# Kernel tuning notes

Measured on AMD Instinct MI355X. Metric: run time of the kernel, lower is better.

Reference implementation:

```python
import jax, jax.numpy as jnp
import numpy as np

N_NODES = 100000
N_EDGES = 1600000
HIDDEN = 128
OUT = 64
NUM_LAYERS = 3


def setup_inputs() -> dict:
    key = jax.random.key(0)
    k1, k2, k3 = jax.random.split(key, 3)
    x = jax.random.normal(k1, (N_NODES, HIDDEN), dtype=jnp.float32)
    edge_index = jax.random.randint(k2, (2, N_EDGES), 0, N_NODES, dtype=jnp.int64)
    W = jax.random.normal(k3, (OUT, HIDDEN), dtype=jnp.float32) * (1.0 / np.sqrt(HIDDEN))
    b = jnp.zeros((OUT,), dtype=jnp.float32)
    return {"x": x, "edge_index": edge_index, "W": W, "b": b}


def reference(x, edge_index, W, b):
    n = x.shape[0]
    row, col = edge_index[0], edge_index[1]
    # degree of destination nodes (bincount over row), clamped to >= 1
    deg = jax.ops.segment_sum(jnp.ones_like(row, dtype=x.dtype), row, num_segments=n)
    deg_inv_sqrt = jnp.clip(deg, 1.0, None) ** -0.5
    norm = (deg_inv_sqrt[row] * deg_inv_sqrt[col])[:, None]  # [E, 1]

    def propagate(h):
        # gather -> scale -> scatter-add
        return jax.ops.segment_sum(h[col] * norm, row, num_segments=n)

    embs = [x]
    h = x
    for _ in range(NUM_LAYERS):
        h = propagate(h)
        embs.append(h)
    out = jnp.mean(jnp.stack(embs, axis=0), axis=0)  # [N, HIDDEN]
    return out @ W.T + b
```

## Files before the change

### kernel.cpp

```cpp
#include <hip/hip_runtime.h>

#define N_NODES 100000
#define N_EDGES 1600000
#define HIDDEN  128
#define OUTF    64
#define SLOT    48

#define EDGE4BLKS ((N_EDGES / 4 + 255) / 256)
#define NODEBLKS  ((N_NODES + 255) / 256)
#define PULLBLKS  ((N_NODES + 15) / 16)

__device__ __forceinline__ unsigned short f2bf(float f) {
    unsigned u = __float_as_uint(f);
    u += 0x7fffu + ((u >> 16) & 1u);
    return (unsigned short)(u >> 16);
}
__device__ __forceinline__ float2 bfp2f(unsigned p) {
    return make_float2(__uint_as_float(p << 16), __uint_as_float(p & 0xffff0000u));
}
__device__ __forceinline__ unsigned packbf(float a, float b) {
    return (unsigned)f2bf(a) | ((unsigned)f2bf(b) << 16);
}

__global__ void prep_kernel(const float* __restrict__ W, float* __restrict__ Wt,
                            int4* __restrict__ cnt4,
                            int4* __restrict__ z0d, int4* __restrict__ z1d,
                            int4* __restrict__ z2d) {
    int bid = blockIdx.x, tid = threadIdx.x;
    if (bid < 98) {
        int i = bid * 256 + tid;
        if (i < N_NODES / 4) cnt4[i] = make_int4(0, 0, 0, 0);
    } else if (bid < 130) {
        int i = (bid - 98) * 256 + tid;
        if (i < HIDDEN * OUTF) {
            int o = i / HIDDEN, k = i % HIDDEN;
            Wt[k * OUTF + o] = W[i];
        }
    } else {
        if (tid < 8)       z0d[tid]      = make_int4(0, 0, 0, 0);
        else if (tid < 16) z1d[tid - 8]  = make_int4(0, 0, 0, 0);
        else if (tid < 24) z2d[tid - 16] = make_int4(0, 0, 0, 0);
    }
}

#define GR    64
#define BK    32
#define HSP   36
#define WTP   68
__global__ __launch_bounds__(256) void mega_a_kernel(const float* __restrict__ x,
                                                     const float* __restrict__ Wt,
                                                     unsigned short* __restrict__ y0,
                                                     const int* __restrict__ ei,
                                                     int* __restrict__ cnt,
                                                     int* __restrict__ rank) {
    __shared__ float hs[GR * HSP];
    __shared__ float wt[BK * WTP];
    int tid = threadIdx.x;

    if (blockIdx.x & 1) {
        int cb = blockIdx.x >> 1;
        int t  = cb * 256 + tid;
        int e0 = t * 4;
        if (e0 + 3 < N_EDGES) {
            int4 r4 = *(const int4*)(ei + e0);
            int k0 = atomicAdd(&cnt[r4.x], 1);
            int k1 = atomicAdd(&cnt[r4.y], 1);
            int k2 = atomicAdd(&cnt[r4.z], 1);
            int k3 = atomicAdd(&cnt[r4.w], 1);
            *(int4*)(rank + e0) = make_int4(k0, k1, k2, k3);
        } else {
            for (int e = e0; e < N_EDGES; ++e) rank[e] = atomicAdd(&cnt[ei[e]], 1);
        }
        return;
    }

    int rowBase = (blockIdx.x >> 1) * GR;
    int o4 = (tid & 15) * 4;
    int rq = (tid >> 4) * 4;
    float4 a0 = {0,0,0,0}, a1 = {0,0,0,0}, a2 = {0,0,0,0}, a3 = {0,0,0,0};

    for (int kt = 0; kt < HIDDEN / BK; ++kt) {
        if (kt) __syncthreads();
        int kbase = kt * BK;
        #pragma unroll
        for (int t = 0; t < 2; ++t) {
            int f = tid + t * 256;
            int r = f >> 3, c4 = (f & 7) * 4;
            int row = rowBase + r;
            float4 v = (row < N_NODES) ? *(const float4*)(x + (size_t)row * HIDDEN + kbase + c4)
                                       : make_float4(0.f, 0.f, 0.f, 0.f);
            *(float4*)&hs[r * HSP + c4] = v;
        }
        #pragma unroll
        for (int t = 0; t < 2; ++t) {
            int f = tid + t * 256;
            int k = f >> 4, c4 = (f & 15) * 4;
            float4 v = *(const float4*)(Wt + (size_t)(kbase + k) * OUTF + c4);
            *(float4*)&wt[k * WTP + c4] = v;
        }
        __syncthreads();
        #pragma unroll 8
        for (int kk = 0; kk < BK; ++kk) {
            float4 wv = *(const float4*)&wt[kk * WTP + o4];
            float h0 = hs[(rq + 0) * HSP + kk];
            float h1 = hs[(rq + 1) * HSP + kk];
            float h2 = hs[(rq + 2) * HSP + kk];
            float h3 = hs[(rq + 3) * HSP + kk];
            a0.x += h0 * wv.x; a0.y += h0 * wv.y; a0.z += h0 * wv.z; a0.w += h0 * wv.w;
            a1.x += h1 * wv.x; a1.y += h1 * wv.y; a1.z += h1 * wv.z; a1.w += h1 * wv.w;
            a2.x += h2 * wv.x; a2.y += h2 * wv.y; a2.z += h2 * wv.z; a2.w += h2 * wv.w;
            a3.x += h3 * wv.x; a3.y += h3 * wv.y; a3.z += h3 * wv.z; a3.w += h3 * wv.w;
        }
    }
    int row = rowBase + rq;
    #pragma unroll
    for (int r = 0; r < 4; ++r) {
        if (row + r < N_NODES) {
            float4 a = (r == 0) ? a0 : (r == 1) ? a1 : (r == 2) ? a2 : a3;
            ushort4 s = {f2bf(a.x), f2bf(a.y), f2bf(a.z), f2bf(a.w)};
            *(ushort4*)&y0[(size_t)(row + r) * OUTF + o4] = s;
        }
    }
}

__global__ void mega_b_kernel(const int* __restrict__ ei,
                              const int* __restrict__ rank,
                              int* __restrict__ csr,
                              const int* __restrict__ cnt,
                              float* __restrict__ dinv,
                              float* __restrict__ rdinv) {
    int bid = blockIdx.x, tid = threadIdx.x;
    if (bid < EDGE4BLKS) {
        int t  = bid * 256 + tid;
        int e0 = t * 4;
        if (e0 + 3 < N_EDGES) {
            int4 r4 = *(const int4*)(ei + e0);
            int4 c4 = *(const int4*)(ei + N_EDGES + e0);
            int4 k4 = *(const int4*)(rank + e0);
            if (k4.x < SLOT) csr[r4.x * SLOT + k4.x] = c4.x;
            if (k4.y < SLOT) csr[r4.y * SLOT + k4.y] = c4.y;
            if (k4.z < SLOT) csr[r4.z * SLOT + k4.z] = c4.z;
            if (k4.w < SLOT) csr[r4.w * SLOT + k4.w] = c4.w;
        } else {
            for (int e = e0; e < N_EDGES; ++e) {
                int k = rank[e];
                if (k < SLOT) csr[ei[e] * SLOT + k] = ei[N_EDGES + e];
            }
        }
    } else {
        int i = (bid - EDGE4BLKS) * 256 + tid;
        if (i < N_NODES) {
            int deg  = cnt[i];
            float d  = fmaxf((float)deg, 1.0f);
            dinv[i]  = rsqrtf(d);
            rdinv[i] = sqrtf(d);
            if (i == 0) dinv[N_NODES] = 0.0f;
            int dc = deg > SLOT ? SLOT : deg;
            int dp = (dc + 7) & ~7;
            #pragma unroll
            for (int j = 0; j < 7; ++j)
                if (dc + j < dp) csr[i * SLOT + dc + j] = N_NODES;
        }
    }
}

template<bool SC>
__global__ __launch_bounds__(256) void pull_v2_kernel(const int* __restrict__ cnt,
                                                      const int* __restrict__ csr,
                                                      const float* __restrict__ dinv,
                                                      const unsigned short* __restrict__ zsrc,
                                                      unsigned short* __restrict__ zdst) {
    int lane = threadIdx.x & 63;
    int wid  = (blockIdx.x * blockDim.x + threadIdx.x) >> 6;
    int g    = lane >> 3;
    int node = wid * 4 + (g >> 1);
    int par  = g & 1;
    int fo   = (lane & 7) * 8;
    bool valid = node < N_NODES;
    int deg = valid ? cnt[node] : 0;
    if (deg > SLOT) deg = SLOT;
    int degp = (deg + 7) & ~7;
    int s = node * SLOT;
    float a0=0.f,a1=0.f,a2=0.f,a3=0.f,a4=0.f,a5=0.f,a6=0.f,a7=0.f;

    int e16 = degp & ~15;
    int i = 0;
    for (; i < e16; i += 16) {
        int c0 = csr[s + i +  0 + par];
        int c1 = csr[s + i +  2 + par];
        int c2 = csr[s + i +  4 + par];
        int c3 = csr[s + i +  6 + par];
        int c4 = csr[s + i +  8 + par];
        int c5 = csr[s + i + 10 + par];
        int c6 = csr[s + i + 12 + par];
        int c7 = csr[s + i + 14 + par];
        float d0=1.f,d1=1.f,d2=1.f,d3=1.f,d4=1.f,d5=1.f,d6=1.f,d7=1.f;
        if (SC) {
            d0 = dinv[c0]; d1 = dinv[c1]; d2 = dinv[c2]; d3 = dinv[c3];
            d4 = dinv[c4]; d5 = dinv[c5]; d6 = dinv[c6]; d7 = dinv[c7];
        }
        uint4 p0 = *(const uint4*)(zsrc + (size_t)c0 * OUTF + fo);
        uint4 p1 = *(const uint4*)(zsrc + (size_t)c1 * OUTF + fo);
        uint4 p2 = *(const uint4*)(zsrc + (size_t)c2 * OUTF + fo);
        uint4 p3 = *(const uint4*)(zsrc + (size_t)c3 * OUTF + fo);
        uint4 p4 = *(const uint4*)(zsrc + (size_t)c4 * OUTF + fo);
        uint4 p5 = *(const uint4*)(zsrc + (size_t)c5 * OUTF + fo);
        uint4 p6 = *(const uint4*)(zsrc + (size_t)c6 * OUTF + fo);
        uint4 p7 = *(const uint4*)(zsrc + (size_t)c7 * OUTF + fo);
        #define ACC(P, D) { \
            float2 q0 = bfp2f(P.x), q1 = bfp2f(P.y), q2 = bfp2f(P.z), q3 = bfp2f(P.w); \
            a0 += D*q0.x; a1 += D*q0.y; a2 += D*q1.x; a3 += D*q1.y; \
            a4 += D*q2.x; a5 += D*q2.y; a6 += D*q3.x; a7 += D*q3.y; }
        ACC(p0, d0) ACC(p1, d1) ACC(p2, d2) ACC(p3, d3)
        ACC(p4, d4) ACC(p5, d5) ACC(p6, d6) ACC(p7, d7)
    }
    if (degp & 8) {
        int c0 = csr[s + i + 0 + par];
        int c1 = csr[s + i + 2 + par];
        int c2 = csr[s + i + 4 + par];
        int c3 = csr[s + i + 6 + par];
        float d0=1.f,d1=1.f,d2=1.f,d3=1.f;
        if (SC) { d0 = dinv[c0]; d1 = dinv[c1]; d2 = dinv[c2]; d3 = dinv[c3]; }
        uint4 p0 = *(const uint4*)(zsrc + (size_t)c0 * OUTF + fo);
        uint4 p1 = *(const uint4*)(zsrc + (size_t)c1 * OUTF + fo);
        uint4 p2 = *(const uint4*)(zsrc + (size_t)c2 * OUTF + fo);
        uint4 p3 = *(const uint4*)(zsrc + (size_t)c3 * OUTF + fo);
        ACC(p0, d0) ACC(p1, d1) ACC(p2, d2) ACC(p3, d3)
        #undef ACC
    }
    a0 += __shfl_xor(a0, 8); a1 += __shfl_xor(a1, 8);
    a2 += __shfl_xor(a2, 8); a3 += __shfl_xor(a3, 8);
    a4 += __shfl_xor(a4, 8); a5 += __shfl_xor(a5, 8);
    a6 += __shfl_xor(a6, 8); a7 += __shfl_xor(a7, 8);
    if ((lane & 8) == 0 && valid) {
        float dn = dinv[node];
        float zs = dn * dn;
        uint4 o;
        o.x = packbf(a0 * zs, a1 * zs);
        o.y = packbf(a2 * zs, a3 * zs);
        o.z = packbf(a4 * zs, a5 * zs);
        o.w = packbf(a6 * zs, a7 * zs);
        *(uint4*)(zdst + (size_t)node * OUTF + fo) = o;
    }
}

__global__ __launch_bounds__(256) void pull_merge_v2_kernel(const int* __restrict__ cnt,
                                                            const int* __restrict__ csr,
                                                            const float* __restrict__ dinv,
                                                            const float* __restrict__ rdinv,
                                                            const unsigned short* __restrict__ y0,
                                                            const unsigned short* __restrict__ z1,
                                                            const unsigned short* __restrict__ z2,
                                                            const float* __restrict__ b,
                                                            float* __restrict__ out) {
    int lane = threadIdx.x & 63;
    int wid  = (blockIdx.x * blockDim.x + threadIdx.x) >> 6;
    int g    = lane >> 3;
    int node = wid * 4 + (g >> 1);
    int par  = g & 1;
    int fo   = (lane & 7) * 8;
    bool valid = node < N_NODES;
    int deg = valid ? cnt[node] : 0;
    if (deg > SLOT) deg = SLOT;
    int degp = (deg + 7) & ~7;
    int s = node * SLOT;
    float a0=0.f,a1=0.f,a2=0.f,a3=0.f,a4=0.f,a5=0.f,a6=0.f,a7=0.f;

    int e16 = degp & ~15;
    int i = 0;
    for (; i < e16; i += 16) {
        int c0 = csr[s + i +  0 + par];
        int c1 = csr[s + i +  2 + par];
        int c2 = csr[s + i +  4 + par];
        int c3 = csr[s + i +  6 + par];
        int c4 = csr[s + i +  8 + par];
        int c5 = csr[s + i + 10 + par];
        int c6 = csr[s + i + 12 + par];
        int c7 = csr[s + i + 14 + par];
        uint4 p0 = *(const uint4*)(z2 + (size_t)c0 * OUTF + fo);
        uint4 p1 = *(const uint4*)(z2 + (size_t)c1 * OUTF + fo);
        uint4 p2 = *(const uint4*)(z2 + (size_t)c2 * OUTF + fo);
        uint4 p3 = *(const uint4*)(z2 + (size_t)c3 * OUTF + fo);
        uint4 p4 = *(const uint4*)(z2 + (size_t)c4 * OUTF + fo);
        uint4 p5 = *(const uint4*)(z2 + (size_t)c5 * OUTF + fo);
        uint4 p6 = *(const uint4*)(z2 + (size_t)c6 * OUTF + fo);
        uint4 p7 = *(const uint4*)(z2 + (size_t)c7 * OUTF + fo);
        #define ACC1(P) { \
            float2 q0 = bfp2f(P.x), q1 = bfp2f(P.y), q2 = bfp2f(P.z), q3 = bfp2f(P.w); \
            a0 += q0.x; a1 += q0.y; a2 += q1.x; a3 += q1.y; \
            a4 += q2.x; a5 += q2.y; a6 += q3.x; a7 += q3.y; }
        ACC1(p0) ACC1(p1) ACC1(p2) ACC1(p3) ACC1(p4) ACC1(p5) ACC1(p6) ACC1(p7)
    }
    if (degp & 8) {
        int c0 = csr[s + i + 0 + par];
        int c1 = csr[s + i + 2 + par];
        int c2 = csr[s + i + 4 + par];
        int c3 = csr[s + i + 6 + par];
        uint4 p0 = *(const uint4*)(z2 + (size_t)c0 * OUTF + fo);
        uint4 p1 = *(const uint4*)(z2 + (size_t)c1 * OUTF + fo);
        uint4 p2 = *(const uint4*)(z2 + (size_t)c2 * OUTF + fo);
        uint4 p3 = *(const uint4*)(z2 + (size_t)c3 * OUTF + fo);
        ACC1(p0) ACC1(p1) ACC1(p2) ACC1(p3)
        #undef ACC1
    }
    a0 += __shfl_xor(a0, 8); a1 += __shfl_xor(a1, 8);
    a2 += __shfl_xor(a2, 8); a3 += __shfl_xor(a3, 8);
    a4 += __shfl_xor(a4, 8); a5 += __shfl_xor(a5, 8);
    a6 += __shfl_xor(a6, 8); a7 += __shfl_xor(a7, 8);
    if ((lane & 8) == 0 && valid) {
        size_t idx = (size_t)node * OUTF + fo;
        float dn = dinv[node];
        float rd = rdinv[node];
        uint4 py = *(const uint4*)(y0 + idx);
        uint4 pz1 = *(const uint4*)(z1 + idx);
        uint4 pz2 = *(const uint4*)(z2 + idx);
        float4 bv0 = *(const float4*)(b + fo);
        float4 bv1 = *(const float4*)(b + fo + 4);
        float2 y_0 = bfp2f(py.x), y_1 = bfp2f(py.y), y_2 = bfp2f(py.z), y_3 = bfp2f(py.w);
        float2 u_0 = bfp2f(pz1.x), u_1 = bfp2f(pz1.y), u_2 = bfp2f(pz1.z), u_3 = bfp2f(pz1.w);
        float2 v_0 = bfp2f(pz2.x), v_1 = bfp2f(pz2.y), v_2 = bfp2f(pz2.z), v_3 = bfp2f(pz2.w);
        float4 r0, r1;
        r0.x = 0.25f * ((dn * y_0.x + u_0.x + v_0.x) * rd + dn * a0) + bv0.x;
        r0.y = 0.25f * ((dn * y_0.y + u_0.y + v_0.y) * rd + dn * a1) + bv0.y;
        r0.z = 0.25f * ((dn * y_1.x + u_1.x + v_1.x) * rd + dn * a2) + bv0.z;
        r0.w = 0.25f * ((dn * y_1.y + u_1.y + v_1.y) * rd + dn * a3) + bv0.w;
        r1.x = 0.25f * ((dn * y_2.x + u_2.x + v_2.x) * rd + dn * a4) + bv1.x;
        r1.y = 0.25f * ((dn * y_2.y + u_2.y + v_2.y) * rd + dn * a5) + bv1.y;
        r1.z = 0.25f * ((dn * y_3.x + u_3.x + v_3.x) * rd + dn * a6) + bv1.z;
        r1.w = 0.25f * ((dn * y_3.y + u_3.y + v_3.y) * rd + dn * a7) + bv1.w;
        *(float4*)(out + idx) = r0;
        *(float4*)(out + idx + 4) = r1;
    }
}

extern "C" void kernel_launch(void* const* d_in, const int* in_sizes, int n_in,
                              void* d_out, int out_size, void* d_ws, size_t ws_size,
                              hipStream_t stream) {
    const float* x  = (const float*)d_in[0];
    const int*   ei = (const int*)d_in[1];
    const float* W  = (const float*)d_in[2];
    const float* b  = (const float*)d_in[3];
    float*       out = (float*)d_out;

    const size_t ZROWS = (size_t)N_NODES + 1;
    unsigned short* y0 = (unsigned short*)d_ws;
    unsigned short* z1 = y0 + ZROWS * OUTF;
    unsigned short* z2 = z1 + ZROWS * OUTF;
    float* Wt      = (float*)(z2 + ZROWS * OUTF);
    int*   csr     = (int*)(Wt + HIDDEN * OUTF);
    int*   cnt     = csr + (size_t)N_NODES * SLOT;
    float* dinv    = (float*)(cnt + N_NODES);
    float* rdinv   = dinv + (N_NODES + 1);

    int* rank = (int*)z2;

    const int BLK = 256;

    prep_kernel<<<131, BLK, 0, stream>>>(W, Wt, (int4*)cnt,
                                         (int4*)(y0 + (size_t)N_NODES * OUTF),
                                         (int4*)(z1 + (size_t)N_NODES * OUTF),
                                         (int4*)(z2 + (size_t)N_NODES * OUTF));
    mega_a_kernel<<<2 * EDGE4BLKS, BLK, 0, stream>>>(x, Wt, y0, ei, cnt, rank);
    mega_b_kernel<<<EDGE4BLKS + NODEBLKS, BLK, 0, stream>>>(ei, rank, csr, cnt, dinv, rdinv);
    pull_v2_kernel<true><<<PULLBLKS, BLK, 0, stream>>>(cnt, csr, dinv, y0, z1);
    pull_v2_kernel<false><<<PULLBLKS, BLK, 0, stream>>>(cnt, csr, dinv, z1, z2);
    pull_merge_v2_kernel<<<PULLBLKS, BLK, 0, stream>>>(cnt, csr, dinv, rdinv,
                                                       y0, z1, z2, b, out);
}
```

Measured before the change: 282.3 us.

## Split feature matrices into 16-column quarter planes for cache-local gathers

Stores the bf16 node feature arrays as four separate planes of 16 features each (32 bytes per row), and launches the pull kernels over four times as many blocks, one feature quarter per block group. Each gather pass then touches a working set a quarter the size, which is meant to fit better in L2/MALL and cut DRAM traffic for random neighbor reads. In exchange the CSR indices and degrees are re-read four times, each gather moves only 32 bytes per row, and the shuffle reduction grows to three steps. The rank scratch now aliases z1 instead of z2, and the first pull kernel re-zeroes the sentinel row of z1 that this aliasing overwrites.

```diff
diff --git a/kernel.cpp b/kernel.cpp
--- a/kernel.cpp
+++ b/kernel.cpp
@@ -8,7 +8,8 @@
 
 #define EDGE4BLKS ((N_EDGES / 4 + 255) / 256)
 #define NODEBLKS  ((N_NODES + 255) / 256)
-#define PULLBLKS  ((N_NODES + 15) / 16)
+#define QSTRIDE ((size_t)(N_NODES + 1) * 16)
+#define T_TILES ((N_NODES + 15) / 16)
 
 __device__ __forceinline__ unsigned short f2bf(float f) {
     unsigned u = __float_as_uint(f);
@@ -24,8 +25,9 @@
 
 __global__ void prep_kernel(const float* __restrict__ W, float* __restrict__ Wt,
                             int4* __restrict__ cnt4,
-                            int4* __restrict__ z0d, int4* __restrict__ z1d,
-                            int4* __restrict__ z2d) {
+                            unsigned short* __restrict__ y0,
+                            unsigned short* __restrict__ z1,
+                            unsigned short* __restrict__ z2) {
     int bid = blockIdx.x, tid = threadIdx.x;
     if (bid < 98) {
         int i = bid * 256 + tid;
@@ -37,9 +39,13 @@
             Wt[k * OUTF + o] = W[i];
         }
     } else {
-        if (tid < 8)       z0d[tid]      = make_int4(0, 0, 0, 0);
-        else if (tid < 16) z1d[tid - 8]  = make_int4(0, 0, 0, 0);
-        else if (tid < 24) z2d[tid - 16] = make_int4(0, 0, 0, 0);
+        if (tid < 24) {
+            unsigned short* base = (tid < 8) ? y0 : (tid < 16) ? z1 : z2;
+            int r = tid & 7;
+            int q = r >> 1, part = r & 1;
+            int4* p = (int4*)(base + q * QSTRIDE + (size_t)N_NODES * 16);
+            p[part] = make_int4(0, 0, 0, 0);
+        }
     }
 }
 
@@ -113,12 +119,14 @@
         }
     }
     int row = rowBase + rq;
+    int q   = o4 >> 4;
+    int off = o4 & 15;
     #pragma unroll
     for (int r = 0; r < 4; ++r) {
         if (row + r < N_NODES) {
             float4 a = (r == 0) ? a0 : (r == 1) ? a1 : (r == 2) ? a2 : a3;
             ushort4 s = {f2bf(a.x), f2bf(a.y), f2bf(a.z), f2bf(a.w)};
-            *(ushort4*)&y0[(size_t)(row + r) * OUTF + o4] = s;
+            *(ushort4*)&y0[q * QSTRIDE + (size_t)(row + r) * 16 + off] = s;
         }
     }
 }
@@ -164,75 +172,62 @@
     }
 }
 
-template<bool SC>
-__global__ __launch_bounds__(256) void pull_v2_kernel(const int* __restrict__ cnt,
-                                                      const int* __restrict__ csr,
-                                                      const float* __restrict__ dinv,
-                                                      const unsigned short* __restrict__ zsrc,
-                                                      unsigned short* __restrict__ zdst) {
+template<bool SC, bool FIXZ>
+__global__ __launch_bounds__(256) void pull_q_kernel(const int* __restrict__ cnt,
+                                                     const int* __restrict__ csr,
+                                                     const float* __restrict__ dinv,
+                                                     const unsigned short* __restrict__ zsrc,
+                                                     unsigned short* __restrict__ zdst) {
+    if (FIXZ && blockIdx.x == 0 && threadIdx.x < 2)
+        ((int4*)(zdst + (size_t)N_NODES * 16))[threadIdx.x] = make_int4(0, 0, 0, 0);
+    int q    = blockIdx.x / T_TILES;
+    int t    = blockIdx.x % T_TILES;
     int lane = threadIdx.x & 63;
-    int wid  = (blockIdx.x * blockDim.x + threadIdx.x) >> 6;
-    int g    = lane >> 3;
-    int node = wid * 4 + (g >> 1);
-    int par  = g & 1;
-    int fo   = (lane & 7) * 8;
+    int wv   = threadIdx.x >> 6;
+    int n    = lane >> 4;
+    int slot = (lane >> 1) & 7;
+    int h    = lane & 1;
+    int node = t * 16 + wv * 4 + n;
     bool valid = node < N_NODES;
     int deg = valid ? cnt[node] : 0;
     if (deg > SLOT) deg = SLOT;
     int degp = (deg + 7) & ~7;
     int s = node * SLOT;
+    const unsigned short* zq = zsrc + q * QSTRIDE;
+    int fo = h * 8;
     float a0=0.f,a1=0.f,a2=0.f,a3=0.f,a4=0.f,a5=0.f,a6=0.f,a7=0.f;
 
     int e16 = degp & ~15;
     int i = 0;
+    #define ACC(P, D) { \
+        float2 q0 = bfp2f(P.x), q1 = bfp2f(P.y), q2 = bfp2f(P.z), q3 = bfp2f(P.w); \
+        a0 += D*q0.x; a1 += D*q0.y; a2 += D*q1.x; a3 += D*q1.y; \
+        a4 += D*q2.x; a5 += D*q2.y; a6 += D*q3.x; a7 += D*q3.y; }
     for (; i < e16; i += 16) {
-        int c0 = csr[s + i +  0 + par];
-        int c1 = csr[s + i +  2 + par];
-        int c2 = csr[s + i +  4 + par];
-        int c3 = csr[s + i +  6 + par];
-        int c4 = csr[s + i +  8 + par];
-        int c5 = csr[s + i + 10 + par];
-        int c6 = csr[s + i + 12 + par];
-        int c7 = csr[s + i + 14 + par];
-        float d0=1.f,d1=1.f,d2=1.f,d3=1.f,d4=1.f,d5=1.f,d6=1.f,d7=1.f;
-        if (SC) {
-            d0 = dinv[c0]; d1 = dinv[c1]; d2 = dinv[c2]; d3 = dinv[c3];
-            d4 = dinv[c4]; d5 = dinv[c5]; d6 = dinv[c6]; d7 = dinv[c7];
-        }
-        uint4 p0 = *(const uint4*)(zsrc + (size_t)c0 * OUTF + fo);
-        uint4 p1 = *(const uint4*)(zsrc + (size_t)c1 * OUTF + fo);
-        uint4 p2 = *(const uint4*)(zsrc + (size_t)c2 * OUTF + fo);
-        uint4 p3 = *(const uint4*)(zsrc + (size_t)c3 * OUTF + fo);
-        uint4 p4 = *(const uint4*)(zsrc + (size_t)c4 * OUTF + fo);
-        uint4 p5 = *(const uint4*)(zsrc + (size_t)c5 * OUTF + fo);
-        uint4 p6 = *(const uint4*)(zsrc + (size_t)c6 * OUTF + fo);
-        uint4 p7 = *(const uint4*)(zsrc + (size_t)c7 * OUTF + fo);
-        #define ACC(P, D) { \
-            float2 q0 = bfp2f(P.x), q1 = bfp2f(P.y), q2 = bfp2f(P.z), q3 = bfp2f(P.w); \
-            a0 += D*q0.x; a1 += D*q0.y; a2 += D*q1.x; a3 += D*q1.y; \
-            a4 += D*q2.x; a5 += D*q2.y; a6 += D*q3.x; a7 += D*q3.y; }
-        ACC(p0, d0) ACC(p1, d1) ACC(p2, d2) ACC(p3, d3)
-        ACC(p4, d4) ACC(p5, d5) ACC(p6, d6) ACC(p7, d7)
+        int c0 = csr[s + i + slot];
+        int c1 = csr[s + i + 8 + slot];
+        float d0 = 1.f, d1 = 1.f;
+        if (SC) { d0 = dinv[c0]; d1 = dinv[c1]; }
+        uint4 p0 = *(const uint4*)(zq + (size_t)c0 * 16 + fo);
+        uint4 p1 = *(const uint4*)(zq + (size_t)c1 * 16 + fo);
+        ACC(p0, d0) ACC(p1, d1)
     }
     if (degp & 8) {
-        int c0 = csr[s + i + 0 + par];
-        int c1 = csr[s + i + 2 + par];
-        int c2 = csr[s + i + 4 + par];
-        int c3 = csr[s + i + 6 + par];
-        float d0=1.f,d1=1.f,d2=1.f,d3=1.f;
-        if (SC) { d0 = dinv[c0]; d1 = dinv[c1]; d2 = dinv[c2]; d3 = dinv[c3]; }
-        uint4 p0 = *(const uint4*)(zsrc + (size_t)c0 * OUTF + fo);
-        uint4 p1 = *(const uint4*)(zsrc + (size_t)c1 * OUTF + fo);
-        uint4 p2 = *(const uint4*)(zsrc + (size_t)c2 * OUTF + fo);
-        uint4 p3 = *(const uint4*)(zsrc + (size_t)c3 * OUTF + fo);
-        ACC(p0, d0) ACC(p1, d1) ACC(p2, d2) ACC(p3, d3)
-        #undef ACC
-    }
-    a0 += __shfl_xor(a0, 8); a1 += __shfl_xor(a1, 8);
-    a2 += __shfl_xor(a2, 8); a3 += __shfl_xor(a3, 8);
-    a4 += __shfl_xor(a4, 8); a5 += __shfl_xor(a5, 8);
-    a6 += __shfl_xor(a6, 8); a7 += __shfl_xor(a7, 8);
-    if ((lane & 8) == 0 && valid) {
+        int c0 = csr[s + i + slot];
+        float d0 = 1.f;
+        if (SC) d0 = dinv[c0];
+        uint4 p0 = *(const uint4*)(zq + (size_t)c0 * 16 + fo);
+        ACC(p0, d0)
+    }
+    #undef ACC
+    #pragma unroll
+    for (int m = 2; m <= 8; m <<= 1) {
+        a0 += __shfl_xor(a0, m); a1 += __shfl_xor(a1, m);
+        a2 += __shfl_xor(a2, m); a3 += __shfl_xor(a3, m);
+        a4 += __shfl_xor(a4, m); a5 += __shfl_xor(a5, m);
+        a6 += __shfl_xor(a6, m); a7 += __shfl_xor(a7, m);
+    }
+    if (slot == 0 && valid) {
         float dn = dinv[node];
         float zs = dn * dn;
         uint4 o;
@@ -240,83 +235,73 @@
         o.y = packbf(a2 * zs, a3 * zs);
         o.z = packbf(a4 * zs, a5 * zs);
         o.w = packbf(a6 * zs, a7 * zs);
-        *(uint4*)(zdst + (size_t)node * OUTF + fo) = o;
-    }
-}
-
-__global__ __launch_bounds__(256) void pull_merge_v2_kernel(const int* __restrict__ cnt,
-                                                            const int* __restrict__ csr,
-                                                            const float* __restrict__ dinv,
-                                                            const float* __restrict__ rdinv,
-                                                            const unsigned short* __restrict__ y0,
-                                                            const unsigned short* __restrict__ z1,
-                                                            const unsigned short* __restrict__ z2,
-                                                            const float* __restrict__ b,
-                                                            float* __restrict__ out) {
+        *(uint4*)(zdst + q * QSTRIDE + (size_t)node * 16 + fo) = o;
+    }
+}
+
+__global__ __launch_bounds__(256) void pull_merge_q_kernel(const int* __restrict__ cnt,
+                                                           const int* __restrict__ csr,
+                                                           const float* __restrict__ dinv,
+                                                           const float* __restrict__ rdinv,
+                                                           const unsigned short* __restrict__ y0,
+                                                           const unsigned short* __restrict__ z1,
+                                                           const unsigned short* __restrict__ z2,
+                                                           const float* __restrict__ b,
+                                                           float* __restrict__ out) {
+    int q    = blockIdx.x / T_TILES;
+    int t    = blockIdx.x % T_TILES;
     int lane = threadIdx.x & 63;
-    int wid  = (blockIdx.x * blockDim.x + threadIdx.x) >> 6;
-    int g    = lane >> 3;
-    int node = wid * 4 + (g >> 1);
-    int par  = g & 1;
-    int fo   = (lane & 7) * 8;
+    int wv   = threadIdx.x >> 6;
+    int n    = lane >> 4;
+    int slot = (lane >> 1) & 7;
+    int h    = lane & 1;
+    int node = t * 16 + wv * 4 + n;
     bool valid = node < N_NODES;
     int deg = valid ? cnt[node] : 0;
     if (deg > SLOT) deg = SLOT;
     int degp = (deg + 7) & ~7;
     int s = node * SLOT;
+    const unsigned short* zq = z2 + q * QSTRIDE;
+    int fo = h * 8;
     float a0=0.f,a1=0.f,a2=0.f,a3=0.f,a4=0.f,a5=0.f,a6=0.f,a7=0.f;
 
     int e16 = degp & ~15;
     int i = 0;
+    #define ACC1(P) { \
+        float2 q0 = bfp2f(P.x), q1 = bfp2f(P.y), q2 = bfp2f(P.z), q3 = bfp2f(P.w); \
+        a0 += q0.x; a1 += q0.y; a2 += q1.x; a3 += q1.y; \
+        a4 += q2.x; a5 += q2.y; a6 += q3.x; a7 += q3.y; }
     for (; i < e16; i += 16) {
-        int c0 = csr[s + i +  0 + par];
-        int c1 = csr[s + i +  2 + par];
-        int c2 = csr[s + i +  4 + par];
-        int c3 = csr[s + i +  6 + par];
-        int c4 = csr[s + i +  8 + par];
-        int c5 = csr[s + i + 10 + par];
-        int c6 = csr[s + i + 12 + par];
-        int c7 = csr[s + i + 14 + par];
-        uint4 p0 = *(const uint4*)(z2 + (size_t)c0 * OUTF + fo);
-        uint4 p1 = *(const uint4*)(z2 + (size_t)c1 * OUTF + fo);
-        uint4 p2 = *(const uint4*)(z2 + (size_t)c2 * OUTF + fo);
-        uint4 p3 = *(const uint4*)(z2 + (size_t)c3 * OUTF + fo);
-        uint4 p4 = *(const uint4*)(z2 + (size_t)c4 * OUTF + fo);
-        uint4 p5 = *(const uint4*)(z2 + (size_t)c5 * OUTF + fo);
-        uint4 p6 = *(const uint4*)(z2 + (size_t)c6 * OUTF + fo);
-        uint4 p7 = *(const uint4*)(z2 + (size_t)c7 * OUTF + fo);
-        #define ACC1(P) { \
-            float2 q0 = bfp2f(P.x), q1 = bfp2f(P.y), q2 = bfp2f(P.z), q3 = bfp2f(P.w); \
-            a0 += q0.x; a1 += q0.y; a2 += q1.x; a3 += q1.y; \
-            a4 += q2.x; a5 += q2.y; a6 += q3.x; a7 += q3.y; }
-        ACC1(p0) ACC1(p1) ACC1(p2) ACC1(p3) ACC1(p4) ACC1(p5) ACC1(p6) ACC1(p7)
+        int c0 = csr[s + i + slot];
+        int c1 = csr[s + i + 8 + slot];
+        uint4 p0 = *(const uint4*)(zq + (size_t)c0 * 16 + fo);
+        uint4 p1 = *(const uint4*)(zq + (size_t)c1 * 16 + fo);
+        ACC1(p0) ACC1(p1)
     }
     if (degp & 8) {
-        int c0 = csr[s + i + 0 + par];
-        int c1 = csr[s + i + 2 + par];
-        int c2 = csr[s + i + 4 + par];
-        int c3 = csr[s + i + 6 + par];
-        uint4 p0 = *(const uint4*)(z2 + (size_t)c0 * OUTF + fo);
-        uint4 p1 = *(const uint4*)(z2 + (size_t)c1 * OUTF + fo);
-        uint4 p2 = *(const uint4*)(z2 + (size_t)c2 * OUTF + fo);
-        uint4 p3 = *(const uint4*)(z2 + (size_t)c3 * OUTF + fo);
-        ACC1(p0) ACC1(p1) ACC1(p2) ACC1(p3)
-        #undef ACC1
-    }
-    a0 += __shfl_xor(a0, 8); a1 += __shfl_xor(a1, 8);
-    a2 += __shfl_xor(a2, 8); a3 += __shfl_xor(a3, 8);
-    a4 += __shfl_xor(a4, 8); a5 += __shfl_xor(a5, 8);
-    a6 += __shfl_xor(a6, 8); a7 += __shfl_xor(a7, 8);
-    if ((lane & 8) == 0 && valid) {
-        size_t idx = (size_t)node * OUTF + fo;
+        int c0 = csr[s + i + slot];
+        uint4 p0 = *(const uint4*)(zq + (size_t)c0 * 16 + fo);
+        ACC1(p0)
+    }
+    #undef ACC1
+    #pragma unroll
+    for (int m = 2; m <= 8; m <<= 1) {
+        a0 += __shfl_xor(a0, m); a1 += __shfl_xor(a1, m);
+        a2 += __shfl_xor(a2, m); a3 += __shfl_xor(a3, m);
+        a4 += __shfl_xor(a4, m); a5 += __shfl_xor(a5, m);
+        a6 += __shfl_xor(a6, m); a7 += __shfl_xor(a7, m);
+    }
+    if (slot == 0 && valid) {
+        size_t idxq = q * QSTRIDE + (size_t)node * 16 + fo;
         float dn = dinv[node];
         float rd = rdinv[node];
-        uint4 py = *(const uint4*)(y0 + idx);
-        uint4 pz1 = *(const uint4*)(z1 + idx);
-        uint4 pz2 = *(const uint4*)(z2 + idx);
-        float4 bv0 = *(const float4*)(b + fo);
-        float4 bv1 = *(const float4*)(b + fo + 4);
-        float2 y_0 = bfp2f(py.x), y_1 = bfp2f(py.y), y_2 = bfp2f(py.z), y_3 = bfp2f(py.w);
+        uint4 py  = *(const uint4*)(y0 + idxq);
+        uint4 pz1 = *(const uint4*)(z1 + idxq);
+        uint4 pz2 = *(const uint4*)(z2 + idxq);
+        int fb = q * 16 + fo;
+        float4 bv0 = *(const float4*)(b + fb);
+        float4 bv1 = *(const float4*)(b + fb + 4);
+        float2 y_0 = bfp2f(py.x),  y_1 = bfp2f(py.y),  y_2 = bfp2f(py.z),  y_3 = bfp2f(py.w);
         float2 u_0 = bfp2f(pz1.x), u_1 = bfp2f(pz1.y), u_2 = bfp2f(pz1.z), u_3 = bfp2f(pz1.w);
         float2 v_0 = bfp2f(pz2.x), v_1 = bfp2f(pz2.y), v_2 = bfp2f(pz2.z), v_3 = bfp2f(pz2.w);
         float4 r0, r1;
@@ -328,8 +313,9 @@
         r1.y = 0.25f * ((dn * y_2.y + u_2.y + v_2.y) * rd + dn * a5) + bv1.y;
         r1.z = 0.25f * ((dn * y_3.x + u_3.x + v_3.x) * rd + dn * a6) + bv1.z;
         r1.w = 0.25f * ((dn * y_3.y + u_3.y + v_3.y) * rd + dn * a7) + bv1.w;
-        *(float4*)(out + idx) = r0;
-        *(float4*)(out + idx + 4) = r1;
+        size_t oi = (size_t)node * OUTF + fb;
+        *(float4*)(out + oi)     = r0;
+        *(float4*)(out + oi + 4) = r1;
     }
 }
 
@@ -342,28 +328,24 @@
     const float* b  = (const float*)d_in[3];
     float*       out = (float*)d_out;
 
-    const size_t ZROWS = (size_t)N_NODES + 1;
     unsigned short* y0 = (unsigned short*)d_ws;
-    unsigned short* z1 = y0 + ZROWS * OUTF;
-    unsigned short* z2 = z1 + ZROWS * OUTF;
-    float* Wt      = (float*)(z2 + ZROWS * OUTF);
+    unsigned short* z1 = y0 + 4 * QSTRIDE;
+    unsigned short* z2 = z1 + 4 * QSTRIDE;
+    float* Wt      = (float*)(z2 + 4 * QSTRIDE);
     int*   csr     = (int*)(Wt + HIDDEN * OUTF);
     int*   cnt     = csr + (size_t)N_NODES * SLOT;
     float* dinv    = (float*)(cnt + N_NODES);
     float* rdinv   = dinv + (N_NODES + 1);
 
-    int* rank = (int*)z2;
+    int* rank = (int*)z1;
 
     const int BLK = 256;
 
-    prep_kernel<<<131, BLK, 0, stream>>>(W, Wt, (int4*)cnt,
-                                         (int4*)(y0 + (size_t)N_NODES * OUTF),
-                                         (int4*)(z1 + (size_t)N_NODES * OUTF),
-                                         (int4*)(z2 + (size_t)N_NODES * OUTF));
+    prep_kernel<<<131, BLK, 0, stream>>>(W, Wt, (int4*)cnt, y0, z1, z2);
     mega_a_kernel<<<2 * EDGE4BLKS, BLK, 0, stream>>>(x, Wt, y0, ei, cnt, rank);
     mega_b_kernel<<<EDGE4BLKS + NODEBLKS, BLK, 0, stream>>>(ei, rank, csr, cnt, dinv, rdinv);
-    pull_v2_kernel<true><<<PULLBLKS, BLK, 0, stream>>>(cnt, csr, dinv, y0, z1);
-    pull_v2_kernel<false><<<PULLBLKS, BLK, 0, stream>>>(cnt, csr, dinv, z1, z2);
-    pull_merge_v2_kernel<<<PULLBLKS, BLK, 0, stream>>>(cnt, csr, dinv, rdinv,
-                                                       y0, z1, z2, b, out);
-}
+    pull_q_kernel<true, true><<<4 * T_TILES, BLK, 0, stream>>>(cnt, csr, dinv, y0, z1);
+    pull_q_kernel<false, false><<<4 * T_TILES, BLK, 0, stream>>>(cnt, csr, dinv, z1, z2);
+    pull_merge_q_kernel<<<4 * T_TILES, BLK, 0, stream>>>(cnt, csr, dinv, rdinv,
+                                                         y0, z1, z2, b, out);
+}
```

Result: slower. 366.4 us (+29.8%).

## Assign two nodes per 8-lane group in pull kernels instead of splitting one node

Applied to the files above, without the earlier changes.

Each 8-lane group now processes two destination nodes with interleaved gathers and no cross-lane reduction, where before two groups split one node's edges by parity. Each thread issues 16 independent row loads per iteration, which raises memory-level parallelism and removes the shuffle reduction. The launch uses a quarter as many blocks. The cost is more registers per thread, possibly lower occupancy, and idle padded loads when the two nodes have unequal degrees.

```diff
diff --git a/kernel.cpp b/kernel.cpp
--- a/kernel.cpp
+++ b/kernel.cpp
@@ -8,7 +8,7 @@
 
 #define EDGE4BLKS ((N_EDGES / 4 + 255) / 256)
 #define NODEBLKS  ((N_NODES + 255) / 256)
-#define PULLBLKS  ((N_NODES + 15) / 16)
+#define PULLBLKS  ((N_NODES + 63) / 64)
 
 __device__ __forceinline__ unsigned short f2bf(float f) {
     unsigned u = __float_as_uint(f);
@@ -165,7 +165,7 @@
 }
 
 template<bool SC>
-__global__ __launch_bounds__(256) void pull_v2_kernel(const int* __restrict__ cnt,
+__global__ __launch_bounds__(256) void pull_v3_kernel(const int* __restrict__ cnt,
                                                       const int* __restrict__ csr,
                                                       const float* __restrict__ dinv,
                                                       const unsigned short* __restrict__ zsrc,
@@ -173,78 +173,93 @@
     int lane = threadIdx.x & 63;
     int wid  = (blockIdx.x * blockDim.x + threadIdx.x) >> 6;
     int g    = lane >> 3;
-    int node = wid * 4 + (g >> 1);
-    int par  = g & 1;
     int fo   = (lane & 7) * 8;
-    bool valid = node < N_NODES;
-    int deg = valid ? cnt[node] : 0;
-    if (deg > SLOT) deg = SLOT;
-    int degp = (deg + 7) & ~7;
-    int s = node * SLOT;
-    float a0=0.f,a1=0.f,a2=0.f,a3=0.f,a4=0.f,a5=0.f,a6=0.f,a7=0.f;
-
-    int e16 = degp & ~15;
-    int i = 0;
-    for (; i < e16; i += 16) {
-        int c0 = csr[s + i +  0 + par];
-        int c1 = csr[s + i +  2 + par];
-        int c2 = csr[s + i +  4 + par];
-        int c3 = csr[s + i +  6 + par];
-        int c4 = csr[s + i +  8 + par];
-        int c5 = csr[s + i + 10 + par];
-        int c6 = csr[s + i + 12 + par];
-        int c7 = csr[s + i + 14 + par];
-        float d0=1.f,d1=1.f,d2=1.f,d3=1.f,d4=1.f,d5=1.f,d6=1.f,d7=1.f;
+    int nodeA = wid * 16 + g * 2;
+    int nodeB = nodeA + 1;
+    bool vA = nodeA < N_NODES, vB = nodeB < N_NODES;
+    int degA = vA ? cnt[nodeA] : 0; if (degA > SLOT) degA = SLOT;
+    int degB = vB ? cnt[nodeB] : 0; if (degB > SLOT) degB = SLOT;
+    int dpA = (degA + 7) & ~7;
+    int dpB = (degB + 7) & ~7;
+    int sA = nodeA * SLOT, sB = nodeB * SLOT;
+    int nIt = (dpA > dpB ? dpA : dpB);
+    float aA0=0.f,aA1=0.f,aA2=0.f,aA3=0.f,aA4=0.f,aA5=0.f,aA6=0.f,aA7=0.f;
+    float aB0=0.f,aB1=0.f,aB2=0.f,aB3=0.f,aB4=0.f,aB5=0.f,aB6=0.f,aB7=0.f;
+
+    for (int j = 0; j < nIt; j += 8) {
+        bool doA = j < dpA, doB = j < dpB;
+        int cA0,cA1,cA2,cA3,cA4,cA5,cA6,cA7;
+        int cB0,cB1,cB2,cB3,cB4,cB5,cB6,cB7;
+        if (doA) {
+            cA0 = csr[sA+j+0]; cA1 = csr[sA+j+1]; cA2 = csr[sA+j+2]; cA3 = csr[sA+j+3];
+            cA4 = csr[sA+j+4]; cA5 = csr[sA+j+5]; cA6 = csr[sA+j+6]; cA7 = csr[sA+j+7];
+        } else { cA0=cA1=cA2=cA3=cA4=cA5=cA6=cA7=N_NODES; }
+        if (doB) {
+            cB0 = csr[sB+j+0]; cB1 = csr[sB+j+1]; cB2 = csr[sB+j+2]; cB3 = csr[sB+j+3];
+            cB4 = csr[sB+j+4]; cB5 = csr[sB+j+5]; cB6 = csr[sB+j+6]; cB7 = csr[sB+j+7];
+        } else { cB0=cB1=cB2=cB3=cB4=cB5=cB6=cB7=N_NODES; }
+        uint4 pA0 = *(const uint4*)(zsrc + (size_t)cA0 * OUTF + fo);
+        uint4 pA1 = *(const uint4*)(zsrc + (size_t)cA1 * OUTF + fo);
+        uint4 pA2 = *(const uint4*)(zsrc + (size_t)cA2 * OUTF + fo);
+        uint4 pA3 = *(const uint4*)(zsrc + (size_t)cA3 * OUTF + fo);
+        uint4 pA4 = *(const uint4*)(zsrc + (size_t)cA4 * OUTF + fo);
+        uint4 pA5 = *(const uint4*)(zsrc + (size_t)cA5 * OUTF + fo);
+        uint4 pA6 = *(const uint4*)(zsrc + (size_t)cA6 * OUTF + fo);
+        uint4 pA7 = *(const uint4*)(zsrc + (size_t)cA7 * OUTF + fo);
+        uint4 pB0 = *(const uint4*)(zsrc + (size_t)cB0 * OUTF + fo);
+        uint4 pB1 = *(const uint4*)(zsrc + (size_t)cB1 * OUTF + fo);
+        uint4 pB2 = *(const uint4*)(zsrc + (size_t)cB2 * OUTF + fo);
+        uint4 pB3 = *(const uint4*)(zsrc + (size_t)cB3 * OUTF + fo);
+        uint4 pB4 = *(const uint4*)(zsrc + (size_t)cB4 * OUTF + fo);
+        uint4 pB5 = *(const uint4*)(zsrc + (size_t)cB5 * OUTF + fo);
+        uint4 pB6 = *(const uint4*)(zsrc + (size_t)cB6 * OUTF + fo);
+        uint4 pB7 = *(const uint4*)(zsrc + (size_t)cB7 * OUTF + fo);
+        float dA0=1.f,dA1=1.f,dA2=1.f,dA3=1.f,dA4=1.f,dA5=1.f,dA6=1.f,dA7=1.f;
+        float dB0=1.f,dB1=1.f,dB2=1.f,dB3=1.f,dB4=1.f,dB5=1.f,dB6=1.f,dB7=1.f;
         if (SC) {
-            d0 = dinv[c0]; d1 = dinv[c1]; d2 = dinv[c2]; d3 = dinv[c3];
-            d4 = dinv[c4]; d5 = dinv[c5]; d6 = dinv[c6]; d7 = dinv[c7];
-        }
-        uint4 p0 = *(const uint4*)(zsrc + (size_t)c0 * OUTF + fo);
-        uint4 p1 = *(const uint4*)(zsrc + (size_t)c1 * OUTF + fo);
-        uint4 p2 = *(const uint4*)(zsrc + (size_t)c2 * OUTF + fo);
-        uint4 p3 = *(const uint4*)(zsrc + (size_t)c3 * OUTF + fo);
-        uint4 p4 = *(const uint4*)(zsrc + (size_t)c4 * OUTF + fo);
-        uint4 p5 = *(const uint4*)(zsrc + (size_t)c5 * OUTF + fo);
-        uint4 p6 = *(const uint4*)(zsrc + (size_t)c6 * OUTF + fo);
-        uint4 p7 = *(const uint4*)(zsrc + (size_t)c7 * OUTF + fo);
-        #define ACC(P, D) { \
+            dA0 = dinv[cA0]; dA1 = dinv[cA1]; dA2 = dinv[cA2]; dA3 = dinv[cA3];
+            dA4 = dinv[cA4]; dA5 = dinv[cA5]; dA6 = dinv[cA6]; dA7 = dinv[cA7];
+            dB0 = dinv[cB0]; dB1 = dinv[cB1]; dB2 = dinv[cB2]; dB3 = dinv[cB3];
+            dB4 = dinv[cB4]; dB5 = dinv[cB5]; dB6 = dinv[cB6]; dB7 = dinv[cB7];
+        }
+        #define ACCA(P, D) { \
             float2 q0 = bfp2f(P.x), q1 = bfp2f(P.y), q2 = bfp2f(P.z), q3 = bfp2f(P.w); \
-            a0 += D*q0.x; a1 += D*q0.y; a2 += D*q1.x; a3 += D*q1.y; \
-            a4 += D*q2.x; a5 += D*q2.y; a6 += D*q3.x; a7 += D*q3.y; }
-        ACC(p0, d0) ACC(p1, d1) ACC(p2, d2) ACC(p3, d3)
-        ACC(p4, d4) ACC(p5, d5) ACC(p6, d6) ACC(p7, d7)
-    }
-    if (degp & 8) {
-        int c0 = csr[s + i + 0 + par];
-        int c1 = csr[s + i + 2 + par];
-        int c2 = csr[s + i + 4 + par];
-        int c3 = csr[s + i + 6 + par];
-        float d0=1.f,d1=1.f,d2=1.f,d3=1.f;
-        if (SC) { d0 = dinv[c0]; d1 = dinv[c1]; d2 = dinv[c2]; d3 = dinv[c3]; }
-        uint4 p0 = *(const uint4*)(zsrc + (size_t)c0 * OUTF + fo);
-        uint4 p1 = *(const uint4*)(zsrc + (size_t)c1 * OUTF + fo);
-        uint4 p2 = *(const uint4*)(zsrc + (size_t)c2 * OUTF + fo);
-        uint4 p3 = *(const uint4*)(zsrc + (size_t)c3 * OUTF + fo);
-        ACC(p0, d0) ACC(p1, d1) ACC(p2, d2) ACC(p3, d3)
-        #undef ACC
-    }
-    a0 += __shfl_xor(a0, 8); a1 += __shfl_xor(a1, 8);
-    a2 += __shfl_xor(a2, 8); a3 += __shfl_xor(a3, 8);
-    a4 += __shfl_xor(a4, 8); a5 += __shfl_xor(a5, 8);
-    a6 += __shfl_xor(a6, 8); a7 += __shfl_xor(a7, 8);
-    if ((lane & 8) == 0 && valid) {
-        float dn = dinv[node];
+            aA0 += D*q0.x; aA1 += D*q0.y; aA2 += D*q1.x; aA3 += D*q1.y; \
+            aA4 += D*q2.x; aA5 += D*q2.y; aA6 += D*q3.x; aA7 += D*q3.y; }
+        #define ACCB(P, D) { \
+            float2 q0 = bfp2f(P.x), q1 = bfp2f(P.y), q2 = bfp2f(P.z), q3 = bfp2f(P.w); \
+            aB0 += D*q0.x; aB1 += D*q0.y; aB2 += D*q1.x; aB3 += D*q1.y; \
+            aB4 += D*q2.x; aB5 += D*q2.y; aB6 += D*q3.x; aB7 += D*q3.y; }
+        ACCA(pA0,dA0) ACCA(pA1,dA1) ACCA(pA2,dA2) ACCA(pA3,dA3)
+        ACCA(pA4,dA4) ACCA(pA5,dA5) ACCA(pA6,dA6) ACCA(pA7,dA7)
+        ACCB(pB0,dB0) ACCB(pB1,dB1) ACCB(pB2,dB2) ACCB(pB3,dB3)
+        ACCB(pB4,dB4) ACCB(pB5,dB5) ACCB(pB6,dB6) ACCB(pB7,dB7)
+        #undef ACCA
+        #undef ACCB
+    }
+    if (vA) {
+        float dn = dinv[nodeA];
         float zs = dn * dn;
         uint4 o;
-        o.x = packbf(a0 * zs, a1 * zs);
-        o.y = packbf(a2 * zs, a3 * zs);
-        o.z = packbf(a4 * zs, a5 * zs);
-        o.w = packbf(a6 * zs, a7 * zs);
-        *(uint4*)(zdst + (size_t)node * OUTF + fo) = o;
-    }
-}
-
-__global__ __launch_bounds__(256) void pull_merge_v2_kernel(const int* __restrict__ cnt,
+        o.x = packbf(aA0 * zs, aA1 * zs);
+        o.y = packbf(aA2 * zs, aA3 * zs);
+        o.z = packbf(aA4 * zs, aA5 * zs);
+        o.w = packbf(aA6 * zs, aA7 * zs);
+        *(uint4*)(zdst + (size_t)nodeA * OUTF + fo) = o;
+    }
+    if (vB) {
+        float dn = dinv[nodeB];
+        float zs = dn * dn;
+        uint4 o;
+        o.x = packbf(aB0 * zs, aB1 * zs);
+        o.y = packbf(aB2 * zs, aB3 * zs);
+        o.z = packbf(aB4 * zs, aB5 * zs);
+        o.w = packbf(aB6 * zs, aB7 * zs);
+        *(uint4*)(zdst + (size_t)nodeB * OUTF + fo) = o;
+    }
+}
+
+__global__ __launch_bounds__(256) void pull_merge_v3_kernel(const int* __restrict__ cnt,
                                                             const int* __restrict__ csr,
                                                             const float* __restrict__ dinv,
                                                             const float* __restrict__ rdinv,
@@ -256,79 +271,108 @@
     int lane = threadIdx.x & 63;
     int wid  = (blockIdx.x * blockDim.x + threadIdx.x) >> 6;
     int g    = lane >> 3;
-    int node = wid * 4 + (g >> 1);
-    int par  = g & 1;
     int fo   = (lane & 7) * 8;
-    bool valid = node < N_NODES;
-    int deg = valid ? cnt[node] : 0;
-    if (deg > SLOT) deg = SLOT;
-    int degp = (deg + 7) & ~7;
-    int s = node * SLOT;
-    float a0=0.f,a1=0.f,a2=0.f,a3=0.f,a4=0.f,a5=0.f,a6=0.f,a7=0.f;
-
-    int e16 = degp & ~15;
-    int i = 0;
-    for (; i < e16; i += 16) {
-        int c0 = csr[s + i +  0 + par];
-        int c1 = csr[s + i +  2 + par];
-        int c2 = csr[s + i +  4 + par];
-        int c3 = csr[s + i +  6 + par];
-        int c4 = csr[s + i +  8 + par];
-        int c5 = csr[s + i + 10 + par];
-        int c6 = csr[s + i + 12 + par];
-        int c7 = csr[s + i + 14 + par];
-        uint4 p0 = *(const uint4*)(z2 + (size_t)c0 * OUTF + fo);
-        uint4 p1 = *(const uint4*)(z2 + (size_t)c1 * OUTF + fo);
-        uint4 p2 = *(const uint4*)(z2 + (size_t)c2 * OUTF + fo);
-        uint4 p3 = *(const uint4*)(z2 + (size_t)c3 * OUTF + fo);
-        uint4 p4 = *(const uint4*)(z2 + (size_t)c4 * OUTF + fo);
-        uint4 p5 = *(const uint4*)(z2 + (size_t)c5 * OUTF + fo);
-        uint4 p6 = *(const uint4*)(z2 + (size_t)c6 * OUTF + fo);
-        uint4 p7 = *(const uint4*)(z2 + (size_t)c7 * OUTF + fo);
-        #define ACC1(P) { \
+    int nodeA = wid * 16 + g * 2;
+    int nodeB = nodeA + 1;
+    bool vA = nodeA < N_NODES, vB = nodeB < N_NODES;
+    int degA = vA ? cnt[nodeA] : 0; if (degA > SLOT) degA = SLOT;
+    int degB = vB ? cnt[nodeB] : 0; if (degB > SLOT) degB = SLOT;
+    int dpA = (degA + 7) & ~7;
+    int dpB = (degB + 7) & ~7;
+    int sA = nodeA * SLOT, sB = nodeB * SLOT;
+    int nIt = (dpA > dpB ? dpA : dpB);
+    float aA0=0.f,aA1=0.f,aA2=0.f,aA3=0.f,aA4=0.f,aA5=0.f,aA6=0.f,aA7=0.f;
+    float aB0=0.f,aB1=0.f,aB2=0.f,aB3=0.f,aB4=0.f,aB5=0.f,aB6=0.f,aB7=0.f;
+
+    for (int j = 0; j < nIt; j += 8) {
+        bool doA = j < dpA, doB = j < dpB;
+        int cA0,cA1,cA2,cA3,cA4,cA5,cA6,cA7;
+        int cB0,cB1,cB2,cB3,cB4,cB5,cB6,cB7;
+        if (doA) {
+            cA0 = csr[sA+j+0]; cA1 = csr[sA+j+1]; cA2 = csr[sA+j+2]; cA3 = csr[sA+j+3];
+            cA4 = csr[sA+j+4]; cA5 = csr[sA+j+5]; cA6 = csr[sA+j+6]; cA7 = csr[sA+j+7];
+        } else { cA0=cA1=cA2=cA3=cA4=cA5=cA6=cA7=N_NODES; }
+        if (doB) {
+            cB0 = csr[sB+j+0]; cB1 = csr[sB+j+1]; cB2 = csr[sB+j+2]; cB3 = csr[sB+j+3];
+            cB4 = csr[sB+j+4]; cB5 = csr[sB+j+5]; cB6 = csr[sB+j+6]; cB7 = csr[sB+j+7];
+        } else { cB0=cB1=cB2=cB3=cB4=cB5=cB6=cB7=N_NODES; }
+        uint4 pA0 = *(const uint4*)(z2 + (size_t)cA0 * OUTF + fo);
+        uint4 pA1 = *(const uint4*)(z2 + (size_t)cA1 * OUTF + fo);
+        uint4 pA2 = *(const uint4*)(z2 + (size_t)cA2 * OUTF + fo);
+        uint4 pA3 = *(const uint4*)(z2 + (size_t)cA3 * OUTF + fo);
+        uint4 pA4 = *(const uint4*)(z2 + (size_t)cA4 * OUTF + fo);
+        uint4 pA5 = *(const uint4*)(z2 + (size_t)cA5 * OUTF + fo);
+        uint4 pA6 = *(const uint4*)(z2 + (size_t)cA6 * OUTF + fo);
+        uint4 pA7 = *(const uint4*)(z2 + (size_t)cA7 * OUTF + fo);
+        uint4 pB0 = *(const uint4*)(z2 + (size_t)cB0 * OUTF + fo);
+        uint4 pB1 = *(const uint4*)(z2 + (size_t)cB1 * OUTF + fo);
+        uint4 pB2 = *(const uint4*)(z2 + (size_t)cB2 * OUTF + fo);
+        uint4 pB3 = *(const uint4*)(z2 + (size_t)cB3 * OUTF + fo);
+        uint4 pB4 = *(const uint4*)(z2 + (size_t)cB4 * OUTF + fo);
+        uint4 pB5 = *(const uint4*)(z2 + (size_t)cB5 * OUTF + fo);
+        uint4 pB6 = *(const uint4*)(z2 + (size_t)cB6 * OUTF + fo);
+        uint4 pB7 = *(const uint4*)(z2 + (size_t)cB7 * OUTF + fo);
+        #define ACCA1(P) { \
             float2 q0 = bfp2f(P.x), q1 = bfp2f(P.y), q2 = bfp2f(P.z), q3 = bfp2f(P.w); \
-            a0 += q0.x; a1 += q0.y; a2 += q1.x; a3 += q1.y; \
-            a4 += q2.x; a5 += q2.y; a6 += q3.x; a7 += q3.y; }
-        ACC1(p0) ACC1(p1) ACC1(p2) ACC1(p3) ACC1(p4) ACC1(p5) ACC1(p6) ACC1(p7)
-    }
-    if (degp & 8) {
-        int c0 = csr[s + i + 0 + par];
-        int c1 = csr[s + i + 2 + par];
-        int c2 = csr[s + i + 4 + par];
-        int c3 = csr[s + i + 6 + par];
-        uint4 p0 = *(const uint4*)(z2 + (size_t)c0 * OUTF + fo);
-        uint4 p1 = *(const uint4*)(z2 + (size_t)c1 * OUTF + fo);
-        uint4 p2 = *(const uint4*)(z2 + (size_t)c2 * OUTF + fo);
-        uint4 p3 = *(const uint4*)(z2 + (size_t)c3 * OUTF + fo);
-        ACC1(p0) ACC1(p1) ACC1(p2) ACC1(p3)
-        #undef ACC1
-    }
-    a0 += __shfl_xor(a0, 8); a1 += __shfl_xor(a1, 8);
-    a2 += __shfl_xor(a2, 8); a3 += __shfl_xor(a3, 8);
-    a4 += __shfl_xor(a4, 8); a5 += __shfl_xor(a5, 8);
-    a6 += __shfl_xor(a6, 8); a7 += __shfl_xor(a7, 8);
-    if ((lane & 8) == 0 && valid) {
-        size_t idx = (size_t)node * OUTF + fo;
-        float dn = dinv[node];
-        float rd = rdinv[node];
-        uint4 py = *(const uint4*)(y0 + idx);
+            aA0 += q0.x; aA1 += q0.y; aA2 += q1.x; aA3 += q1.y; \
+            aA4 += q2.x; aA5 += q2.y; aA6 += q3.x; aA7 += q3.y; }
+        #define ACCB1(P) { \
+            float2 q0 = bfp2f(P.x), q1 = bfp2f(P.y), q2 = bfp2f(P.z), q3 = bfp2f(P.w); \
+            aB0 += q0.x; aB1 += q0.y; aB2 += q1.x; aB3 += q1.y; \
+            aB4 += q2.x; aB5 += q2.y; aB6 += q3.x; aB7 += q3.y; }
+        ACCA1(pA0) ACCA1(pA1) ACCA1(pA2) ACCA1(pA3)
+        ACCA1(pA4) ACCA1(pA5) ACCA1(pA6) ACCA1(pA7)
+        ACCB1(pB0) ACCB1(pB1) ACCB1(pB2) ACCB1(pB3)
+        ACCB1(pB4) ACCB1(pB5) ACCB1(pB6) ACCB1(pB7)
+        #undef ACCA1
+        #undef ACCB1
+    }
+    if (vA) {
+        size_t idx = (size_t)nodeA * OUTF + fo;
+        float dn = dinv[nodeA];
+        float rd = rdinv[nodeA];
+        uint4 py  = *(const uint4*)(y0 + idx);
         uint4 pz1 = *(const uint4*)(z1 + idx);
         uint4 pz2 = *(const uint4*)(z2 + idx);
         float4 bv0 = *(const float4*)(b + fo);
         float4 bv1 = *(const float4*)(b + fo + 4);
-        float2 y_0 = bfp2f(py.x), y_1 = bfp2f(py.y), y_2 = bfp2f(py.z), y_3 = bfp2f(py.w);
+        float2 y_0 = bfp2f(py.x),  y_1 = bfp2f(py.y),  y_2 = bfp2f(py.z),  y_3 = bfp2f(py.w);
         float2 u_0 = bfp2f(pz1.x), u_1 = bfp2f(pz1.y), u_2 = bfp2f(pz1.z), u_3 = bfp2f(pz1.w);
         float2 v_0 = bfp2f(pz2.x), v_1 = bfp2f(pz2.y), v_2 = bfp2f(pz2.z), v_3 = bfp2f(pz2.w);
         float4 r0, r1;
-        r0.x = 0.25f * ((dn * y_0.x + u_0.x + v_0.x) * rd + dn * a0) + bv0.x;
-        r0.y = 0.25f * ((dn * y_0.y + u_0.y + v_0.y) * rd + dn * a1) + bv0.y;
-        r0.z = 0.25f * ((dn * y_1.x + u_1.x + v_1.x) * rd + dn * a2) + bv0.z;
-        r0.w = 0.25f * ((dn * y_1.y + u_1.y + v_1.y) * rd + dn * a3) + bv0.w;
-        r1.x = 0.25f * ((dn * y_2.x + u_2.x + v_2.x) * rd + dn * a4) + bv1.x;
-        r1.y = 0.25f * ((dn * y_2.y + u_2.y + v_2.y) * rd + dn * a5) + bv1.y;
-        r1.z = 0.25f * ((dn * y_3.x + u_3.x + v_3.x) * rd + dn * a6) + bv1.z;
-        r1.w = 0.25f * ((dn * y_3.y + u_3.y + v_3.y) * rd + dn * a7) + bv1.w;
-        *(float4*)(out + idx) = r0;
+        r0.x = 0.25f * ((dn * y_0.x + u_0.x + v_0.x) * rd + dn * aA0) + bv0.x;
+        r0.y = 0.25f * ((dn * y_0.y + u_0.y + v_0.y) * rd + dn * aA1) + bv0.y;
+        r0.z = 0.25f * ((dn * y_1.x + u_1.x + v_1.x) * rd + dn * aA2) + bv0.z;
+        r0.w = 0.25f * ((dn * y_1.y + u_1.y + v_1.y) * rd + dn * aA3) + bv0.w;
+        r1.x = 0.25f * ((dn * y_2.x + u_2.x + v_2.x) * rd + dn * aA4) + bv1.x;
+        r1.y = 0.25f * ((dn * y_2.y + u_2.y + v_2.y) * rd + dn * aA5) + bv1.y;
+        r1.z = 0.25f * ((dn * y_3.x + u_3.x + v_3.x) * rd + dn * aA6) + bv1.z;
+        r1.w = 0.25f * ((dn * y_3.y + u_3.y + v_3.y) * rd + dn * aA7) + bv1.w;
+        *(float4*)(out + idx)     = r0;
+        *(float4*)(out + idx + 4) = r1;
+    }
+    if (vB) {
+        size_t idx = (size_t)nodeB * OUTF + fo;
+        float dn = dinv[nodeB];
+        float rd = rdinv[nodeB];
+        uint4 py  = *(const uint4*)(y0 + idx);
+        uint4 pz1 = *(const uint4*)(z1 + idx);
+        uint4 pz2 = *(const uint4*)(z2 + idx);
+        float4 bv0 = *(const float4*)(b + fo);
+        float4 bv1 = *(const float4*)(b + fo + 4);
+        float2 y_0 = bfp2f(py.x),  y_1 = bfp2f(py.y),  y_2 = bfp2f(py.z),  y_3 = bfp2f(py.w);
+        float2 u_0 = bfp2f(pz1.x), u_1 = bfp2f(pz1.y), u_2 = bfp2f(pz1.z), u_3 = bfp2f(pz1.w);
+        float2 v_0 = bfp2f(pz2.x), v_1 = bfp2f(pz2.y), v_2 = bfp2f(pz2.z), v_3 = bfp2f(pz2.w);
+        float4 r0, r1;
+        r0.x = 0.25f * ((dn * y_0.x + u_0.x + v_0.x) * rd + dn * aB0) + bv0.x;
+        r0.y = 0.25f * ((dn * y_0.y + u_0.y + v_0.y) * rd + dn * aB1) + bv0.y;
+        r0.z = 0.25f * ((dn * y_1.x + u_1.x + v_1.x) * rd + dn * aB2) + bv0.z;
+        r0.w = 0.25f * ((dn * y_1.y + u_1.y + v_1.y) * rd + dn * aB3) + bv0.w;
+        r1.x = 0.25f * ((dn * y_2.x + u_2.x + v_2.x) * rd + dn * aB4) + bv1.x;
+        r1.y = 0.25f * ((dn * y_2.y + u_2.y + v_2.y) * rd + dn * aB5) + bv1.y;
+        r1.z = 0.25f * ((dn * y_3.x + u_3.x + v_3.x) * rd + dn * aB6) + bv1.z;
+        r1.w = 0.25f * ((dn * y_3.y + u_3.y + v_3.y) * rd + dn * aB7) + bv1.w;
+        *(float4*)(out + idx)     = r0;
         *(float4*)(out + idx + 4) = r1;
     }
 }
@@ -362,8 +406,8 @@
                                          (int4*)(z2 + (size_t)N_NODES * OUTF));
     mega_a_kernel<<<2 * EDGE4BLKS, BLK, 0, stream>>>(x, Wt, y0, ei, cnt, rank);
     mega_b_kernel<<<EDGE4BLKS + NODEBLKS, BLK, 0, stream>>>(ei, rank, csr, cnt, dinv, rdinv);
-    pull_v2_kernel<true><<<PULLBLKS, BLK, 0, stream>>>(cnt, csr, dinv, y0, z1);
-    pull_v2_kernel<false><<<PULLBLKS, BLK, 0, stream>>>(cnt, csr, dinv, z1, z2);
-    pull_merge_v2_kernel<<<PULLBLKS, BLK, 0, stream>>>(cnt, csr, dinv, rdinv,
+    pull_v3_kernel<true><<<PULLBLKS, BLK, 0, stream>>>(cnt, csr, dinv, y0, z1);
+    pull_v3_kernel<false><<<PULLBLKS, BLK, 0, stream>>>(cnt, csr, dinv, z1, z2);
+    pull_merge_v3_kernel<<<PULLBLKS, BLK, 0, stream>>>(cnt, csr, dinv, rdinv,
                                                        y0, z1, z2, b, out);
 }
```

Result: slower. 296.3 us (+4.9%).
